# Kernel optimization log

Hardware: AMD Instinct MI355X
Metric: run time of the kernel (lower is better)

## Reference

```python
import jax, jax.numpy as jnp
import numpy as np

N_NODES = 100000
N_EDGES = 1600000
IN_C = 64
HID_C = 2 * IN_C  # 128
OUT_C = 64


def setup_inputs() -> dict:
    key = jax.random.key(0)
    k1, k2, k3, k4 = jax.random.split(key, 4)
    x = jax.random.normal(k1, (N_NODES, IN_C), dtype=jnp.float32)
    edge_index = jax.random.randint(k2, (2, N_EDGES), 0, N_NODES, dtype=jnp.int64)
    # Glorot-ish scaled weights
    W3 = jax.random.normal(k3, (IN_C, HID_C), dtype=jnp.float32) / np.sqrt(IN_C)
    b3 = jnp.zeros((HID_C,), dtype=jnp.float32)
    W4 = jax.random.normal(k4, (HID_C, OUT_C), dtype=jnp.float32) / np.sqrt(HID_C)
    b4 = jnp.zeros((OUT_C,), dtype=jnp.float32)
    return {"x": x, "edge_index": edge_index, "W3": W3, "b3": b3, "W4": W4, "b4": b4}


def _gcn_conv(x, src, dst, norm, W, b, n_nodes):
    # linear transform first (PyG GCNConv: lin then propagate), then
    # degree-normalized gather-scatter aggregation, then bias.
    h = x @ W                              # [N, C_out]
    msg = h[src] * norm[:, None]           # [E+N, C_out] gathered messages
    out = jax.ops.segment_sum(msg, dst, num_segments=n_nodes)
    return out + b


def reference(x, edge_index, W3, b3, W4, b4):
    n_nodes = x.shape[0]
    # add self-loops (PyG GCNConv default add_self_loops=True)
    loops = jnp.arange(n_nodes, dtype=edge_index.dtype)
    src = jnp.concatenate([edge_index[0], loops])  # [E+N]
    dst = jnp.concatenate([edge_index[1], loops])  # [E+N]
    # symmetric normalization: deg over target column incl. self-loops
    deg = jax.ops.segment_sum(jnp.ones(dst.shape, dtype=x.dtype), dst, num_segments=n_nodes)
    dinv = jnp.where(deg > 0, jax.lax.rsqrt(deg), jnp.zeros_like(deg))
    norm = dinv[src] * dinv[dst]                   # [E+N]
    h = jax.nn.relu(_gcn_conv(x, src, dst, norm, W3, b3, n_nodes))
    return _gcn_conv(h, src, dst, norm, W4, b4, n_nodes)
```

## Files before the change

### kernel.cpp

```cpp
#include <hip/hip_runtime.h>
#include <hip/hip_bf16.h>
#include <hip/hip_fp16.h>


constexpr int IN_C  = 64;
constexpr int HID_C = 128;
constexpr int OUT_C = 64;
constexpr int BSHIFT = 9;
constexpr int BW     = 1 << BSHIFT;
constexpr int TILE   = 4096;
constexpr int FCAP   = 16384;

typedef _Float16 f16x8 __attribute__((ext_vector_type(8)));
typedef float    f32x4 __attribute__((ext_vector_type(4)));
typedef int      i32x4 __attribute__((ext_vector_type(4)));

union FragU { uint4 u; f16x8 h; _Float16 q[8]; };

__device__ __forceinline__ f32x4 mfma16(f16x8 a, f16x8 b, f32x4 c) {
    return __builtin_amdgcn_mfma_f32_16x16x32_f16(a, b, c, 0, 0, 0);
}

__device__ __forceinline__ float2 up2(unsigned u) {
    __half2 h = *reinterpret_cast<__half2*>(&u);
    return __half22float2(h);
}
__device__ __forceinline__ unsigned pk2(float a, float b) {
    __half2 h = __float22half2_rn(make_float2(a, b));
    return *reinterpret_cast<unsigned*>(&h);
}

__global__ __launch_bounds__(256) void zero_small_kernel(int* __restrict__ p, int m)
{
    int i = blockIdx.x * 256 + threadIdx.x;
    if (i < m) p[i] = 0;
}

__global__ __launch_bounds__(256) void wfrag_kernel(
    const float* __restrict__ W3, const float* __restrict__ W4,
    uint4* __restrict__ w3f, uint4* __restrict__ w4f)
{
    const int idx = blockIdx.x * 256 + threadIdx.x;
    const int l = idx & 63, cl = l & 15, ch = l >> 4;
    if (idx < 2048) {
        const int fi = idx >> 6;
        const int h = fi & 1, s = (fi >> 1) & 1, c = fi >> 2;
        const int k0 = s * 32 + ch * 8, col = c * 16 + cl;
        FragU f;
        #pragma unroll
        for (int i = 0; i < 8; ++i) {
            float x = W3[(k0 + i) * HID_C + col];
            _Float16 hi = (_Float16)x;
            f.q[i] = h ? (_Float16)(x - (float)hi) : hi;
        }
        w3f[fi * 64 + l] = f.u;
    } else if (idx < 3072) {
        const int fi = (idx - 2048) >> 6;
        const int s = fi & 3, c = fi >> 2;
        const int k0 = s * 32 + ch * 8, col = c * 16 + cl;
        FragU f;
        #pragma unroll
        for (int i = 0; i < 8; ++i)
            f.q[i] = (_Float16)W4[(k0 + i) * OUT_C + col];
        w4f[fi * 64 + l] = f.u;
    }
}

__global__ __launch_bounds__(256) void bhist_kernel(
    const int* __restrict__ dst, int* __restrict__ bcnt, int E, int nbkt)
{
    __shared__ int h[256];
    h[threadIdx.x] = 0;
    __syncthreads();
    const int gid = blockIdx.x * 256 + threadIdx.x;
    const int stride = gridDim.x * 256;
    const int E4 = E >> 2;
    const i32x4* d4p = (const i32x4*)dst;
    for (int e = gid; e < E4; e += stride) {
        i32x4 d4 = __builtin_nontemporal_load(&d4p[e]);
        atomicAdd(&h[d4.x >> BSHIFT], 1);
        atomicAdd(&h[d4.y >> BSHIFT], 1);
        atomicAdd(&h[d4.z >> BSHIFT], 1);
        atomicAdd(&h[d4.w >> BSHIFT], 1);
    }
    if (gid < (E & 3)) {
        int d = dst[E4 * 4 + gid];
        atomicAdd(&h[d >> BSHIFT], 1);
    }
    __syncthreads();
    if (threadIdx.x < nbkt && h[threadIdx.x] != 0)
        atomicAdd(&bcnt[threadIdx.x], h[threadIdx.x]);
}

__global__ __launch_bounds__(256) void bscan_kernel(
    const int* __restrict__ bcnt, int* __restrict__ bbase,
    int* __restrict__ bcur, int nbkt)
{
    __shared__ int s[256];
    int v = (threadIdx.x < nbkt) ? bcnt[threadIdx.x] : 0;
    s[threadIdx.x] = v;
    __syncthreads();
    for (int off = 1; off < 256; off <<= 1) {
        int t = (threadIdx.x >= off) ? s[threadIdx.x - off] : 0;
        __syncthreads();
        s[threadIdx.x] += t;
        __syncthreads();
    }
    if (threadIdx.x < nbkt) {
        int ex = s[threadIdx.x] - v;
        bbase[threadIdx.x] = ex;
        bcur[threadIdx.x]  = ex;
        if (threadIdx.x == nbkt - 1) bbase[nbkt] = s[threadIdx.x];
    }
}

__global__ __launch_bounds__(256) void bin_kernel(
    const int* __restrict__ src, const int* __restrict__ dst,
    int* __restrict__ bcur, unsigned* __restrict__ ebuf, int E, int nbkt)
{
    __shared__ unsigned stageS[TILE];
    __shared__ unsigned char stageB[TILE];
    __shared__ int lcnt[256], lofs[256], lpos[256], gbase[256], s[256];
    const int base = blockIdx.x * TILE;
    const int cnt_mine = min(TILE, E - base);
    const int t = threadIdx.x;
    lcnt[t] = 0;
    __syncthreads();
    unsigned w[16]; int p[16];
    if (base + TILE <= E) {
        const i32x4* s4p = (const i32x4*)(src + base);
        const i32x4* d4p = (const i32x4*)(dst + base);
        #pragma unroll
        for (int k4 = 0; k4 < 4; ++k4) {
            i32x4 s4 = __builtin_nontemporal_load(&s4p[t + k4 * 256]);
            i32x4 d4 = __builtin_nontemporal_load(&d4p[t + k4 * 256]);
            #pragma unroll
            for (int j = 0; j < 4; ++j) {
                int k = k4 * 4 + j;
                int sv = (j == 0) ? s4.x : (j == 1) ? s4.y : (j == 2) ? s4.z : s4.w;
                int dv = (j == 0) ? d4.x : (j == 1) ? d4.y : (j == 2) ? d4.z : d4.w;
                p[k] = dv >> BSHIFT;
                w[k] = ((unsigned)sv << BSHIFT) | (unsigned)(dv & (BW - 1));
                atomicAdd(&lcnt[p[k]], 1);
            }
        }
    } else {
        #pragma unroll
        for (int k = 0; k < 16; ++k) {
            int jo = t + k * 256;
            if (jo < cnt_mine) {
                int sv = __builtin_nontemporal_load(&src[base + jo]);
                int dv = __builtin_nontemporal_load(&dst[base + jo]);
                p[k] = dv >> BSHIFT;
                w[k] = ((unsigned)sv << BSHIFT) | (unsigned)(dv & (BW - 1));
                atomicAdd(&lcnt[p[k]], 1);
            } else p[k] = -1;
        }
    }
    __syncthreads();
    int v = lcnt[t];
    s[t] = v;
    __syncthreads();
    for (int off = 1; off < 256; off <<= 1) {
        int u = (t >= off) ? s[t - off] : 0;
        __syncthreads();
        s[t] += u;
        __syncthreads();
    }
    lofs[t] = s[t] - v;
    lpos[t] = s[t] - v;
    if (t < nbkt && v != 0) gbase[t] = atomicAdd(&bcur[t], v);
    __syncthreads();
    #pragma unroll
    for (int k = 0; k < 16; ++k) {
        if (p[k] >= 0) {
            int pos = atomicAdd(&lpos[p[k]], 1);
            stageS[pos] = w[k];
            stageB[pos] = (unsigned char)p[k];
        }
    }
    __syncthreads();
    for (int j = t; j < cnt_mine; j += 256) {
        int b = stageB[j];
        ebuf[gbase[b] + (j - lofs[b])] = stageS[j];
    }
}

__global__ __launch_bounds__(256) void bucket_kernel(
    const unsigned* __restrict__ ebuf, const int* __restrict__ bbase,
    int* __restrict__ row_start, float* __restrict__ dinv,
    int* __restrict__ sorted_src, int n, int E, int nbkt)
{
    __shared__ int lcnt[BW];
    __shared__ int lcur[BW];
    __shared__ int s[256];
    __shared__ int lsrc[FCAP];
    const int b   = blockIdx.x;
    const int lo  = b << BSHIFT;
    const int hi  = min(lo + BW, n);
    const int nn  = hi - lo;
    const int beg = bbase[b], end = bbase[b + 1];
    const int cnt = end - beg;
    const int t   = threadIdx.x;
    for (int i = t; i < nn; i += 256) lcnt[i] = 0;
    __syncthreads();
    for (int j = beg + t; j < end; j += 256)
        atomicAdd(&lcnt[ebuf[j] & (BW - 1)], 1);
    __syncthreads();
    int a0 = (2 * t     < nn) ? lcnt[2 * t]     : 0;
    int a1 = (2 * t + 1 < nn) ? lcnt[2 * t + 1] : 0;
    int tsum = a0 + a1;
    s[t] = tsum;
    __syncthreads();
    for (int off = 1; off < 256; off <<= 1) {
        int v = (t >= off) ? s[t - off] : 0;
        __syncthreads();
        s[t] += v;
        __syncthreads();
    }
    int texcl = s[t] - tsum;
    if (2 * t < nn) {
        lcur[2 * t] = texcl;
        row_start[lo + 2 * t] = beg + texcl;
        dinv[lo + 2 * t] = rsqrtf((float)a0 + 1.0f);
    }
    if (2 * t + 1 < nn) {
        lcur[2 * t + 1] = texcl + a0;
        row_start[lo + 2 * t + 1] = beg + texcl + a0;
        dinv[lo + 2 * t + 1] = rsqrtf((float)a1 + 1.0f);
    }
    if (t == 0 && b == nbkt - 1) row_start[n] = E;
    __syncthreads();
    if (cnt <= FCAP) {
        for (int j = beg + t; j < end; j += 256) {
            unsigned w = ebuf[j];
            int pos = atomicAdd(&lcur[w & (BW - 1)], 1);
            lsrc[pos] = (int)(w >> BSHIFT);
        }
        __syncthreads();
        for (int j = t; j < cnt; j += 256)
            sorted_src[beg + j] = lsrc[j];
    } else {
        for (int j = beg + t; j < end; j += 256) {
            unsigned w = ebuf[j];
            int pos = atomicAdd(&lcur[w & (BW - 1)], 1);
            sorted_src[beg + pos] = (int)(w >> BSHIFT);
        }
    }
}

__global__ __launch_bounds__(256) void cvt_scaled_kernel(
    const float2* __restrict__ in, const float* __restrict__ dinv,
    unsigned* __restrict__ outw, int nw)
{
    int i = blockIdx.x * 256 + threadIdx.x;
    if (i < nw) {
        float2 v = in[i];
        float dv = dinv[i >> 5];
        outw[i] = pk2(v.x * dv, v.y * dv);
    }
}

template <bool OUT_F16, bool ADD_BIAS>
__global__ __launch_bounds__(256) void agg_f16_kernel(
    const unsigned* __restrict__ feat, const int* __restrict__ row_start,
    const int* __restrict__ sorted_src, const float* __restrict__ dinv,
    const float* __restrict__ bias, void* __restrict__ outp, int n)
{
    const int g  = threadIdx.x >> 3;
    const int gl = threadIdx.x & 7;
    const int d  = blockIdx.x * 32 + g;
    if (d >= n) return;
    const float di = dinv[d];
    const uint4* f4 = (const uint4*)feat;

    float a0x, a0y, a1x, a1y, a2x, a2y, a3x, a3y;
    {
        uint4 u = f4[(size_t)d * 8 + gl];
        float2 f0 = up2(u.x), f1 = up2(u.y), f2 = up2(u.z), f3 = up2(u.w);
        a0x = f0.x; a0y = f0.y; a1x = f1.x; a1y = f1.y;
        a2x = f2.x; a2y = f2.y; a3x = f3.x; a3y = f3.y;
    }

#define ACC(U) do { \
        float2 f0_ = up2((U).x), f1_ = up2((U).y), f2_ = up2((U).z), f3_ = up2((U).w); \
        a0x += f0_.x; a0y += f0_.y; a1x += f1_.x; a1y += f1_.y; \
        a2x += f2_.x; a2y += f2_.y; a3x += f3_.x; a3y += f3_.y; } while (0)
#define LDIDX(v0, v1, v2, v3, at) do { \
        v0 = __builtin_nontemporal_load(&sorted_src[(at)]); \
        v1 = __builtin_nontemporal_load(&sorted_src[min((at) + 1, last)]); \
        v2 = __builtin_nontemporal_load(&sorted_src[min((at) + 2, last)]); \
        v3 = __builtin_nontemporal_load(&sorted_src[min((at) + 3, last)]); } while (0)

    const int beg = row_start[d], end = row_start[d + 1];
    const int last = end - 1;
    int i = beg;
    int ia0 = 0, ia1 = 0, ia2 = 0, ia3 = 0;
    int ib0 = 0, ib1 = 0, ib2 = 0, ib3 = 0;
    uint4 uA0, uA1, uA2, uA3, uB0, uB1, uB2, uB3;
    if (i < end) {
        LDIDX(ia0, ia1, ia2, ia3, i);
        uA0 = f4[(size_t)ia0 * 8 + gl];
        uA1 = f4[(size_t)ia1 * 8 + gl];
        uA2 = f4[(size_t)ia2 * 8 + gl];
        uA3 = f4[(size_t)ia3 * 8 + gl];
        if (i + 4 < end) LDIDX(ib0, ib1, ib2, ib3, i + 4);
    }
    while (i < end) {
        int ni = i + 4;
        if (ni < end) {
            uB0 = f4[(size_t)ib0 * 8 + gl];
            uB1 = f4[(size_t)ib1 * 8 + gl];
            uB2 = f4[(size_t)ib2 * 8 + gl];
            uB3 = f4[(size_t)ib3 * 8 + gl];
        }
        int nn2 = ni + 4;
        if (nn2 < end) LDIDX(ia0, ia1, ia2, ia3, nn2);
        {
            int nb = end - i;
            ACC(uA0);
            if (nb > 1) ACC(uA1);
            if (nb > 2) ACC(uA2);
            if (nb > 3) ACC(uA3);
        }
        i = ni;
        if (i >= end) break;
        ni = i + 4;
        if (ni < end) {
            uA0 = f4[(size_t)ia0 * 8 + gl];
            uA1 = f4[(size_t)ia1 * 8 + gl];
            uA2 = f4[(size_t)ia2 * 8 + gl];
            uA3 = f4[(size_t)ia3 * 8 + gl];
        }
        nn2 = ni + 4;
        if (nn2 < end) LDIDX(ib0, ib1, ib2, ib3, nn2);
        {
            int nb = end - i;
            ACC(uB0);
            if (nb > 1) ACC(uB1);
            if (nb > 2) ACC(uB2);
            if (nb > 3) ACC(uB3);
        }
        i = ni;
    }
#undef ACC
#undef LDIDX

    a0x *= di; a0y *= di; a1x *= di; a1y *= di;
    a2x *= di; a2y *= di; a3x *= di; a3y *= di;
    if (ADD_BIAS) {
        const float4 b0 = ((const float4*)bias)[gl * 2];
        const float4 b1 = ((const float4*)bias)[gl * 2 + 1];
        a0x += b0.x; a0y += b0.y; a1x += b0.z; a1y += b0.w;
        a2x += b1.x; a2y += b1.y; a3x += b1.z; a3y += b1.w;
    }
    if (OUT_F16) {
        uint4 o;
        o.x = pk2(a0x, a0y); o.y = pk2(a1x, a1y);
        o.z = pk2(a2x, a2y); o.w = pk2(a3x, a3y);
        ((uint4*)outp)[(size_t)d * 8 + gl] = o;
    } else {
        float4* op = (float4*)outp;
        op[(size_t)d * 16 + gl * 2]     = make_float4(a0x, a0y, a1x, a1y);
        op[(size_t)d * 16 + gl * 2 + 1] = make_float4(a2x, a2y, a3x, a3y);
    }
}

__global__ __launch_bounds__(256) void gemm12_kernel(
    const unsigned* __restrict__ ax, const uint4* __restrict__ w3f,
    const uint4* __restrict__ w4f, const float* __restrict__ b3,
    const float* __restrict__ dinv, unsigned* __restrict__ t, int n)
{
    __shared__ __align__(16) char lds[32768];
    const int l  = threadIdx.x & 63;
    const int wv = threadIdx.x >> 6;
    const int cl = l & 15, ch = l >> 4;
    const int r0 = blockIdx.x * 128 + wv * 32;

    FragU a1[2][2];
    const uint4* ax4 = (const uint4*)ax;
    #pragma unroll
    for (int rt = 0; rt < 2; ++rt)
        #pragma unroll
        for (int s = 0; s < 2; ++s)
            a1[rt][s].u = ax4[(size_t)(r0 + rt * 16 + cl) * 8 + s * 4 + ch];

    float bb[8];
    #pragma unroll
    for (int c = 0; c < 8; ++c) bb[c] = b3[c * 16 + cl];

    const f32x4 z4 = {0.f, 0.f, 0.f, 0.f};
    f32x4 acc1[2][8];
    #pragma unroll
    for (int rt = 0; rt < 2; ++rt)
        #pragma unroll
        for (int c = 0; c < 8; ++c) acc1[rt][c] = z4;

    #pragma unroll
    for (int c = 0; c < 8; ++c) {
        FragU bh0, bl0, bh1, bl1;
        bh0.u = w3f[(c * 4 + 0) * 64 + l];
        bl0.u = w3f[(c * 4 + 1) * 64 + l];
        bh1.u = w3f[(c * 4 + 2) * 64 + l];
        bl1.u = w3f[(c * 4 + 3) * 64 + l];
        #pragma unroll
        for (int rt = 0; rt < 2; ++rt) {
            f32x4 a = acc1[rt][c];
            a = mfma16(a1[rt][0].h, bh0.h, a);
            a = mfma16(a1[rt][0].h, bl0.h, a);
            a = mfma16(a1[rt][1].h, bh1.h, a);
            a = mfma16(a1[rt][1].h, bl1.h, a);
            acc1[rt][c] = a;
        }
    }

    #pragma unroll
    for (int rt = 0; rt < 2; ++rt) {
        const int tb = (wv * 2 + rt) * 4096;
        #pragma unroll
        for (int c = 0; c < 8; ++c)
            #pragma unroll
            for (int i = 0; i < 4; ++i) {
                int row = ch * 4 + i;
                int off = tb + ((row * 256 + (c * 16 + cl) * 2) ^ ((row & 7) << 4));
                *(_Float16*)&lds[off] =
                    (_Float16)fmaxf(acc1[rt][c][i] + bb[c], 0.0f);
            }
    }

    float dv[2][4];
    #pragma unroll
    for (int rt = 0; rt < 2; ++rt)
        #pragma unroll
        for (int i = 0; i < 4; ++i)
            dv[rt][i] = dinv[min(r0 + rt * 16 + ch * 4 + i, n - 1)];

    FragU a2[2][4];
    #pragma unroll
    for (int rt = 0; rt < 2; ++rt) {
        const int tb = (wv * 2 + rt) * 4096;
        #pragma unroll
        for (int s2 = 0; s2 < 4; ++s2) {
            int off = tb + ((cl * 256 + s2 * 64 + ch * 16) ^ ((cl & 7) << 4));
            a2[rt][s2].u = *(const uint4*)&lds[off];
        }
    }

    f32x4 acc2[2][4];
    #pragma unroll
    for (int rt = 0; rt < 2; ++rt)
        #pragma unroll
        for (int c2 = 0; c2 < 4; ++c2) acc2[rt][c2] = z4;

    #pragma unroll
    for (int c2 = 0; c2 < 4; ++c2)
        #pragma unroll
        for (int s2 = 0; s2 < 4; ++s2) {
            FragU b2; b2.u = w4f[(c2 * 4 + s2) * 64 + l];
            acc2[0][c2] = mfma16(a2[0][s2].h, b2.h, acc2[0][c2]);
            acc2[1][c2] = mfma16(a2[1][s2].h, b2.h, acc2[1][c2]);
        }

    _Float16* th = (_Float16*)t;
    #pragma unroll
    for (int rt = 0; rt < 2; ++rt)
        #pragma unroll
        for (int i = 0; i < 4; ++i) {
            int row = r0 + rt * 16 + ch * 4 + i;
            if (row < n) {
                #pragma unroll
                for (int c2 = 0; c2 < 4; ++c2)
                    th[(size_t)row * 64 + c2 * 16 + cl] =
                        (_Float16)(acc2[rt][c2][i] * dv[rt][i]);
            }
        }
}

extern "C" void kernel_launch(void* const* d_in, const int* in_sizes, int n_in,
                              void* d_out, int out_size, void* d_ws, size_t ws_size,
                              hipStream_t stream)
{
    const float* x  = (const float*)d_in[0];
    const int*   ei = (const int*)d_in[1];
    const float* W3 = (const float*)d_in[2];
    const float* b3 = (const float*)d_in[3];
    const float* W4 = (const float*)d_in[4];
    const float* b4 = (const float*)d_in[5];
    float* out = (float*)d_out;

    const int n = in_sizes[0] / IN_C;
    const int E = in_sizes[1] / 2;
    const int* src = ei;
    const int* dst = ei + E;
    const int nbkt = (n + BW - 1) >> BSHIFT;

    const size_t n_pad = ((size_t)n + 256) & ~(size_t)255;

    int*      bcnt      = (int*)d_ws;
    int*      bbase     = bcnt + 256;
    int*      bcur      = bbase + 512;
    int*      row_start = bcur + 256;
    float*    dinv      = (float*)(row_start + n_pad);
    int*      ssrc      = (int*)(dinv + n_pad);
    unsigned* ebuf      = (unsigned*)(ssrc + (((size_t)E + 255) & ~(size_t)255));
    unsigned* xh        = ebuf + (((size_t)E + 255) & ~(size_t)255);
    unsigned* agg_x     = xh + n_pad * 32;
    uint4*    w3f       = (uint4*)(agg_x + n_pad * 32);
    uint4*    w4f       = w3f + 2048;
    unsigned* t         = xh;

    zero_small_kernel<<<1, 256, 0, stream>>>(bcnt, 256);
    wfrag_kernel<<<12, 256, 0, stream>>>(W3, W4, w3f, w4f);
    bhist_kernel<<<256, 256, 0, stream>>>(dst, bcnt, E, nbkt);
    bscan_kernel<<<1, 256, 0, stream>>>(bcnt, bbase, bcur, nbkt);

    bin_kernel<<<(E + TILE - 1) / TILE, 256, 0, stream>>>(src, dst, bcur, ebuf, E, nbkt);
    bucket_kernel<<<nbkt, 256, 0, stream>>>(ebuf, bbase, row_start, dinv, ssrc, n, E, nbkt);

    cvt_scaled_kernel<<<(n * 32 + 255) / 256, 256, 0, stream>>>(
        (const float2*)x, dinv, xh, n * 32);

    agg_f16_kernel<true, false><<<(n + 31) / 32, 256, 0, stream>>>(
        xh, row_start, ssrc, dinv, nullptr, agg_x, n);

    gemm12_kernel<<<(n + 127) / 128, 256, 0, stream>>>(
        agg_x, w3f, w4f, b3, dinv, t, n);

    agg_f16_kernel<false, true><<<(n + 31) / 32, 256, 0, stream>>>(
        t, row_start, ssrc, dinv, b4, out, n);
}
```

Measured before the change: 229.7 us.

## Fuse first aggregation into GEMM kernel and fold conversion into bucketing

Merges the first sparse aggregation into the GEMM kernel: each block aggregates its 128 rows into swizzled LDS and feeds them straight to the MFMA stage, so the agg_x intermediate never goes through global memory. The dinv-scaled fp16 conversion of x moves into the bucket kernel, which already holds per-node degree counts. The bcnt zeroing is folded into wfrag_kernel. Together these drop three launches and one full-size write and read, at the cost of a heavier fused kernel whose gather latency may be harder to hide and whose occupancy is capped by launch bounds and 32KB of LDS.

```diff
diff --git a/kernel.cpp b/kernel.cpp
--- a/kernel.cpp
+++ b/kernel.cpp
@@ -30,17 +30,12 @@
     return *reinterpret_cast<unsigned*>(&h);
 }
 
-__global__ __launch_bounds__(256) void zero_small_kernel(int* __restrict__ p, int m)
-{
-    int i = blockIdx.x * 256 + threadIdx.x;
-    if (i < m) p[i] = 0;
-}
-
 __global__ __launch_bounds__(256) void wfrag_kernel(
     const float* __restrict__ W3, const float* __restrict__ W4,
-    uint4* __restrict__ w3f, uint4* __restrict__ w4f)
+    uint4* __restrict__ w3f, uint4* __restrict__ w4f, int* __restrict__ bcnt)
 {
     const int idx = blockIdx.x * 256 + threadIdx.x;
+    if (blockIdx.x == 11) bcnt[threadIdx.x] = 0;
     const int l = idx & 63, cl = l & 15, ch = l >> 4;
     if (idx < 2048) {
         const int fi = idx >> 6;
@@ -189,7 +184,8 @@
 __global__ __launch_bounds__(256) void bucket_kernel(
     const unsigned* __restrict__ ebuf, const int* __restrict__ bbase,
     int* __restrict__ row_start, float* __restrict__ dinv,
-    int* __restrict__ sorted_src, int n, int E, int nbkt)
+    int* __restrict__ sorted_src, const float2* __restrict__ x,
+    unsigned* __restrict__ xh, int n, int E, int nbkt)
 {
     __shared__ int lcnt[BW];
     __shared__ int lcur[BW];
@@ -247,25 +243,18 @@
             sorted_src[beg + pos] = (int)(w >> BSHIFT);
         }
     }
-}
-
-__global__ __launch_bounds__(256) void cvt_scaled_kernel(
-    const float2* __restrict__ in, const float* __restrict__ dinv,
-    unsigned* __restrict__ outw, int nw)
-{
-    int i = blockIdx.x * 256 + threadIdx.x;
-    if (i < nw) {
-        float2 v = in[i];
-        float dv = dinv[i >> 5];
-        outw[i] = pk2(v.x * dv, v.y * dv);
-    }
-}
-
-template <bool OUT_F16, bool ADD_BIAS>
-__global__ __launch_bounds__(256) void agg_f16_kernel(
+    for (int j = t; j < nn * 32; j += 256) {
+        int row = j >> 5;
+        float dv = rsqrtf((float)lcnt[row] + 1.0f);
+        float2 v = x[(size_t)(lo + row) * 32 + (j & 31)];
+        xh[(size_t)(lo + row) * 32 + (j & 31)] = pk2(v.x * dv, v.y * dv);
+    }
+}
+
+__global__ __launch_bounds__(256) void agg_out_kernel(
     const unsigned* __restrict__ feat, const int* __restrict__ row_start,
     const int* __restrict__ sorted_src, const float* __restrict__ dinv,
-    const float* __restrict__ bias, void* __restrict__ outp, int n)
+    const float* __restrict__ bias, float* __restrict__ outp, int n)
 {
     const int g  = threadIdx.x >> 3;
     const int gl = threadIdx.x & 7;
@@ -348,42 +337,126 @@
 
     a0x *= di; a0y *= di; a1x *= di; a1y *= di;
     a2x *= di; a2y *= di; a3x *= di; a3y *= di;
-    if (ADD_BIAS) {
-        const float4 b0 = ((const float4*)bias)[gl * 2];
-        const float4 b1 = ((const float4*)bias)[gl * 2 + 1];
-        a0x += b0.x; a0y += b0.y; a1x += b0.z; a1y += b0.w;
-        a2x += b1.x; a2y += b1.y; a3x += b1.z; a3y += b1.w;
-    }
-    if (OUT_F16) {
-        uint4 o;
-        o.x = pk2(a0x, a0y); o.y = pk2(a1x, a1y);
-        o.z = pk2(a2x, a2y); o.w = pk2(a3x, a3y);
-        ((uint4*)outp)[(size_t)d * 8 + gl] = o;
-    } else {
-        float4* op = (float4*)outp;
-        op[(size_t)d * 16 + gl * 2]     = make_float4(a0x, a0y, a1x, a1y);
-        op[(size_t)d * 16 + gl * 2 + 1] = make_float4(a2x, a2y, a3x, a3y);
-    }
-}
-
-__global__ __launch_bounds__(256) void gemm12_kernel(
-    const unsigned* __restrict__ ax, const uint4* __restrict__ w3f,
-    const uint4* __restrict__ w4f, const float* __restrict__ b3,
-    const float* __restrict__ dinv, unsigned* __restrict__ t, int n)
+    const float4 b0 = ((const float4*)bias)[gl * 2];
+    const float4 b1 = ((const float4*)bias)[gl * 2 + 1];
+    a0x += b0.x; a0y += b0.y; a1x += b0.z; a1y += b0.w;
+    a2x += b1.x; a2y += b1.y; a3x += b1.z; a3y += b1.w;
+    float4* op = (float4*)outp;
+    op[(size_t)d * 16 + gl * 2]     = make_float4(a0x, a0y, a1x, a1y);
+    op[(size_t)d * 16 + gl * 2 + 1] = make_float4(a2x, a2y, a3x, a3y);
+}
+
+__global__ __launch_bounds__(256, 4) void aggemm12_kernel(
+    const unsigned* __restrict__ feat, const int* __restrict__ row_start,
+    const int* __restrict__ sorted_src, const float* __restrict__ dinv,
+    const uint4* __restrict__ w3f, const uint4* __restrict__ w4f,
+    const float* __restrict__ b3, unsigned* __restrict__ t, int n)
 {
     __shared__ __align__(16) char lds[32768];
     const int l  = threadIdx.x & 63;
     const int wv = threadIdx.x >> 6;
     const int cl = l & 15, ch = l >> 4;
-    const int r0 = blockIdx.x * 128 + wv * 32;
-
+    const int g  = threadIdx.x >> 3;
+    const int gl = threadIdx.x & 7;
+    const int base = blockIdx.x * 128;
+    const uint4* f4 = (const uint4*)feat;
+
+    #pragma unroll 1
+    for (int pass = 0; pass < 4; ++pass) {
+        const int lr = pass * 32 + g;
+        const int d  = base + lr;
+        uint4 o = make_uint4(0u, 0u, 0u, 0u);
+        if (d < n) {
+            const float di = dinv[d];
+            float a0x, a0y, a1x, a1y, a2x, a2y, a3x, a3y;
+            {
+                uint4 u = f4[(size_t)d * 8 + gl];
+                float2 f0 = up2(u.x), f1 = up2(u.y), f2 = up2(u.z), f3 = up2(u.w);
+                a0x = f0.x; a0y = f0.y; a1x = f1.x; a1y = f1.y;
+                a2x = f2.x; a2y = f2.y; a3x = f3.x; a3y = f3.y;
+            }
+#define ACC(U) do { \
+            float2 f0_ = up2((U).x), f1_ = up2((U).y), f2_ = up2((U).z), f3_ = up2((U).w); \
+            a0x += f0_.x; a0y += f0_.y; a1x += f1_.x; a1y += f1_.y; \
+            a2x += f2_.x; a2y += f2_.y; a3x += f3_.x; a3y += f3_.y; } while (0)
+#define LDIDX(v0, v1, v2, v3, at) do { \
+            v0 = __builtin_nontemporal_load(&sorted_src[(at)]); \
+            v1 = __builtin_nontemporal_load(&sorted_src[min((at) + 1, last)]); \
+            v2 = __builtin_nontemporal_load(&sorted_src[min((at) + 2, last)]); \
+            v3 = __builtin_nontemporal_load(&sorted_src[min((at) + 3, last)]); } while (0)
+            const int beg = row_start[d], end = row_start[d + 1];
+            const int last = end - 1;
+            int i = beg;
+            int ia0 = 0, ia1 = 0, ia2 = 0, ia3 = 0;
+            int ib0 = 0, ib1 = 0, ib2 = 0, ib3 = 0;
+            uint4 uA0, uA1, uA2, uA3, uB0, uB1, uB2, uB3;
+            if (i < end) {
+                LDIDX(ia0, ia1, ia2, ia3, i);
+                uA0 = f4[(size_t)ia0 * 8 + gl];
+                uA1 = f4[(size_t)ia1 * 8 + gl];
+                uA2 = f4[(size_t)ia2 * 8 + gl];
+                uA3 = f4[(size_t)ia3 * 8 + gl];
+                if (i + 4 < end) LDIDX(ib0, ib1, ib2, ib3, i + 4);
+            }
+            while (i < end) {
+                int ni = i + 4;
+                if (ni < end) {
+                    uB0 = f4[(size_t)ib0 * 8 + gl];
+                    uB1 = f4[(size_t)ib1 * 8 + gl];
+                    uB2 = f4[(size_t)ib2 * 8 + gl];
+                    uB3 = f4[(size_t)ib3 * 8 + gl];
+                }
+                int nn2 = ni + 4;
+                if (nn2 < end) LDIDX(ia0, ia1, ia2, ia3, nn2);
+                {
+                    int nb = end - i;
+                    ACC(uA0);
+                    if (nb > 1) ACC(uA1);
+                    if (nb > 2) ACC(uA2);
+                    if (nb > 3) ACC(uA3);
+                }
+                i = ni;
+                if (i >= end) break;
+                ni = i + 4;
+                if (ni < end) {
+                    uA0 = f4[(size_t)ia0 * 8 + gl];
+                    uA1 = f4[(size_t)ia1 * 8 + gl];
+                    uA2 = f4[(size_t)ia2 * 8 + gl];
+                    uA3 = f4[(size_t)ia3 * 8 + gl];
+                }
+                nn2 = ni + 4;
+                if (nn2 < end) LDIDX(ib0, ib1, ib2, ib3, nn2);
+                {
+                    int nb = end - i;
+                    ACC(uB0);
+                    if (nb > 1) ACC(uB1);
+                    if (nb > 2) ACC(uB2);
+                    if (nb > 3) ACC(uB3);
+                }
+                i = ni;
+            }
+#undef ACC
+#undef LDIDX
+            a0x *= di; a0y *= di; a1x *= di; a1y *= di;
+            a2x *= di; a2y *= di; a3x *= di; a3y *= di;
+            o.x = pk2(a0x, a0y); o.y = pk2(a1x, a1y);
+            o.z = pk2(a2x, a2y); o.w = pk2(a3x, a3y);
+        }
+        *(uint4*)&lds[lr * 128 + ((gl * 16) ^ ((lr & 7) << 4))] = o;
+    }
+    __syncthreads();
+
+    const int r0 = base + wv * 32;
     FragU a1[2][2];
-    const uint4* ax4 = (const uint4*)ax;
     #pragma unroll
     for (int rt = 0; rt < 2; ++rt)
         #pragma unroll
-        for (int s = 0; s < 2; ++s)
-            a1[rt][s].u = ax4[(size_t)(r0 + rt * 16 + cl) * 8 + s * 4 + ch];
+        for (int s = 0; s < 2; ++s) {
+            int row = wv * 32 + rt * 16 + cl;
+            a1[rt][s].u = *(const uint4*)&lds[
+                row * 128 + (((s * 4 + ch) * 16) ^ ((row & 7) << 4))];
+        }
+    __syncthreads();
 
     float bb[8];
     #pragma unroll
@@ -504,28 +577,21 @@
     int*      ssrc      = (int*)(dinv + n_pad);
     unsigned* ebuf      = (unsigned*)(ssrc + (((size_t)E + 255) & ~(size_t)255));
     unsigned* xh        = ebuf + (((size_t)E + 255) & ~(size_t)255);
-    unsigned* agg_x     = xh + n_pad * 32;
-    uint4*    w3f       = (uint4*)(agg_x + n_pad * 32);
+    uint4*    w3f       = (uint4*)(xh + n_pad * 32);
     uint4*    w4f       = w3f + 2048;
-    unsigned* t         = xh;
-
-    zero_small_kernel<<<1, 256, 0, stream>>>(bcnt, 256);
-    wfrag_kernel<<<12, 256, 0, stream>>>(W3, W4, w3f, w4f);
+    unsigned* t         = (unsigned*)(w4f + 1024);
+
+    wfrag_kernel<<<12, 256, 0, stream>>>(W3, W4, w3f, w4f, bcnt);
     bhist_kernel<<<256, 256, 0, stream>>>(dst, bcnt, E, nbkt);
     bscan_kernel<<<1, 256, 0, stream>>>(bcnt, bbase, bcur, nbkt);
 
     bin_kernel<<<(E + TILE - 1) / TILE, 256, 0, stream>>>(src, dst, bcur, ebuf, E, nbkt);
-    bucket_kernel<<<nbkt, 256, 0, stream>>>(ebuf, bbase, row_start, dinv, ssrc, n, E, nbkt);
-
-    cvt_scaled_kernel<<<(n * 32 + 255) / 256, 256, 0, stream>>>(
-        (const float2*)x, dinv, xh, n * 32);
-
-    agg_f16_kernel<true, false><<<(n + 31) / 32, 256, 0, stream>>>(
-        xh, row_start, ssrc, dinv, nullptr, agg_x, n);
-
-    gemm12_kernel<<<(n + 127) / 128, 256, 0, stream>>>(
-        agg_x, w3f, w4f, b3, dinv, t, n);
-
-    agg_f16_kernel<false, true><<<(n + 31) / 32, 256, 0, stream>>>(
+    bucket_kernel<<<nbkt, 256, 0, stream>>>(
+        ebuf, bbase, row_start, dinv, ssrc, (const float2*)x, xh, n, E, nbkt);
+
+    aggemm12_kernel<<<(n + 127) / 128, 256, 0, stream>>>(
+        xh, row_start, ssrc, dinv, w3f, w4f, b3, t, n);
+
+    agg_out_kernel<<<(n + 31) / 32, 256, 0, stream>>>(
         t, row_start, ssrc, dinv, b4, out, n);
 }
```

After: 239.4 us. 1.04x slower.
